# Kernel optimization log

Measured on AMD Instinct MI355X. Metric: run time of the kernel, lower is better.

## Reference

```python
import jax, jax.numpy as jnp
import numpy as np

N_NODES = 100000
N_EDGES = 1200000
D_IN = 64
H1 = 64
H2 = 64
N_CLASSES = 40
K_HOPS = 3  # PyG TAGConv default K=3


def _gcn_norm(edge_index, num_nodes):
    # TAGConv uses gcn_norm WITHOUT adding self-loops.
    src, dst = edge_index[0], edge_index[1]
    ones = jnp.ones((src.shape[0],), dtype=jnp.float32)
    deg = jax.ops.segment_sum(ones, dst, num_segments=num_nodes)
    deg_inv_sqrt = jnp.where(deg > 0, jax.lax.rsqrt(jnp.maximum(deg, 1.0)), 0.0)
    return deg_inv_sqrt[src] * deg_inv_sqrt[dst]  # [E]


def _tag_conv(x, src, dst, norm, W, b, num_nodes, K):
    # out = concat([x, Ax, ..., A^K x]) @ W + b, A = D^-1/2 A D^-1/2
    hops = [x]
    h = x
    for _ in range(K):
        h = jax.ops.segment_sum(h[src] * norm[:, None], dst, num_segments=num_nodes)
        hops.append(h)
    return jnp.concatenate(hops, axis=-1) @ W + b


def setup_inputs() -> dict:
    key = jax.random.key(0)
    ks = jax.random.split(key, 9)
    x = jax.random.normal(ks[0], (N_NODES, D_IN), dtype=jnp.float32)
    edge_index = jax.random.randint(ks[1], (2, N_EDGES), 0, N_NODES, dtype=jnp.int64)
    W1 = jax.random.normal(ks[2], ((K_HOPS + 1) * D_IN, H1), dtype=jnp.float32) * 0.05
    b1 = jnp.zeros((H1,), dtype=jnp.float32)
    W2 = jax.random.normal(ks[3], ((K_HOPS + 1) * H1, H2), dtype=jnp.float32) * 0.05
    b2 = jnp.zeros((H2,), dtype=jnp.float32)
    Wc = jax.random.normal(ks[4], (H2, N_CLASSES), dtype=jnp.float32) * 0.05
    bc = jnp.zeros((N_CLASSES,), dtype=jnp.float32)
    return {"x": x, "edge_index": edge_index, "W1": W1, "b1": b1,
            "W2": W2, "b2": b2, "Wc": Wc, "bc": bc}


def reference(x, edge_index, W1, b1, W2, b2, Wc, bc):
    num_nodes = x.shape[0]
    src, dst = edge_index[0], edge_index[1]
    norm = _gcn_norm(edge_index, num_nodes)
    h = _tag_conv(x, src, dst, norm, W1, b1, num_nodes, K_HOPS)
    h = jax.nn.relu(h)  # dropout is identity at inference
    h = _tag_conv(h, src, dst, norm, W2, b2, num_nodes, K_HOPS)
    h = jax.nn.relu(h)
    return h @ Wc + bc  # [N, num_classes]
```

## Files before the change

kernel.cpp:

```cpp
#include <hip/hip_runtime.h>
#include <hip/hip_bf16.h>
#include <stdint.h>

static constexpr int TG_NN = 100000;
static constexpr int TG_NE = 1200000;
static constexpr int TG_D  = 64;
static constexpr int TG_NC = 40;
static constexpr int TG_BT = 256;
static constexpr int TG_GN = (TG_NN + TG_BT - 1) / TG_BT;
static constexpr int TG_CAP = 64;
static constexpr int TG_WSH = 15;
static constexpr int TG_NPASS = (TG_NN + (1 << TG_WSH) - 1) >> TG_WSH;
static constexpr int TG_NR = TG_NN + 128;
static constexpr long TG_BS = (long)TG_NR * TG_D;

typedef __attribute__((ext_vector_type(8))) short tg71_s8;
typedef __attribute__((ext_vector_type(4))) float tg71_f4;

__device__ __forceinline__ float tg71_b2f(unsigned short u) {
    return __uint_as_float(((unsigned int)u) << 16);
}
__device__ __forceinline__ unsigned short tg71_f2b(float v) {
    __hip_bfloat16 b = __float2bfloat16(v);
    return __builtin_bit_cast(unsigned short, b);
}
__device__ __forceinline__ float tg71_ld(const void* p, long i, int isF32) {
    if (isF32) return ((const float*)p)[i];
    return tg71_b2f(((const unsigned short*)p)[i]);
}
__device__ __forceinline__ void tg71_st(void* p, long i, int isF32, float v) {
    if (isF32) ((float*)p)[i] = v;
    else ((unsigned short*)p)[i] = tg71_f2b(v);
}
__device__ __forceinline__ float4 tg71_u2f4(ushort4 u) {
    return float4{tg71_b2f(u.x), tg71_b2f(u.y), tg71_b2f(u.z), tg71_b2f(u.w)};
}

__global__ void tg71_detect(const int* ei, const unsigned short* w1bits, int* flags) {
    int lane = threadIdx.x;
    int hi = ei[2 * lane + 1];
    unsigned long long bi = __ballot(hi != 0);
    float mx = 0.0f;
    for (int k = lane; k < 2048; k += 64) {
        float v = fabsf(tg71_b2f(w1bits[k]));
        if (!(v == v)) v = 1e30f;
        mx = fmaxf(mx, v);
    }
    unsigned long long bf = __ballot(mx > 1e4f);
    if (lane == 0) { flags[0] = (bi == 0ULL) ? 1 : 0; flags[1] = (bf != 0ULL) ? 1 : 0; }
}

extern "C" __global__ void TAGModel_71227737636876_kernel(void* out, const int* flags) {
    long i = (long)blockIdx.x * blockDim.x + threadIdx.x;
    if (i < (long)TG_NN * TG_NC) tg71_st(out, i, flags[1], 123.0f);
}

__global__ void tg71_prep(const void* W1, const void* W2, const int* flags,
                          unsigned short* Wt1, unsigned short* Wt2, int* cnt,
                          unsigned short* Sall) {
    int b = blockIdx.x;
    if (b < 128) {
        const void* W = (b < 64) ? W1 : W2;
        unsigned short* Wt = (b < 64) ? Wt1 : Wt2;
        int i = (b & 63) * TG_BT + threadIdx.x;
        int k = i >> 6, n = i & 63;
        Wt[n * 256 + k] = flags[1] ? tg71_f2b(((const float*)W)[i]) : ((const unsigned short*)W)[i];
    } else if (b < 128 + TG_GN) {
        int i = (b - 128) * TG_BT + threadIdx.x;
        if (i < TG_NN) cnt[i] = 0;
    } else {
        int j = (b - 128 - TG_GN) * TG_BT + threadIdx.x;
        if (j < 5 * 2048) {
            int buf = j >> 11, w = j & 2047;
            unsigned short* base = Sall + (long)buf * TG_BS + (long)TG_NN * TG_D;
            ((uint2*)base)[w] = uint2{0u, 0u};
        }
    }
}

__global__ void tg71_scatter(const int* __restrict__ ei, const int* flags,
                             int* __restrict__ srcI, int* __restrict__ dstI,
                             int* cnt, int* __restrict__ srcS, int pass, int decode) {
    int e = blockIdx.x * blockDim.x + threadIdx.x;
    if (e >= TG_NE) return;
    int s, d;
    if (decode) {
        if (flags[0]) { s = ((const int2*)ei)[e].x; d = ((const int2*)ei)[TG_NE + e].x; }
        else          { s = ei[e]; d = ei[TG_NE + e]; }
        srcI[e] = s;
        dstI[e] = d;
    } else {
        s = srcI[e];
        d = dstI[e];
    }
    if ((d >> TG_WSH) != pass) return;
    int pos = atomicAdd(cnt + d, 1);
    if (pos < TG_CAP) srcS[(d << 6) + pos] = s;
}

__global__ void tg71_gx(const void* x, const int* flags, const int* __restrict__ cnt,
                        float* __restrict__ dis, unsigned short* __restrict__ g) {
    int tid = blockIdx.x * blockDim.x + threadIdx.x;
    if (tid >= TG_NN * 4) return;
    int n = tid >> 2, q = tid & 3;
    if (q == 0) {
        int c = cnt[n];
        dis[n] = c > 0 ? rsqrtf((float)c) : 0.f;
    }
    unsigned short* dst = g + (long)n * TG_D + q * 16;
    if (flags[1]) {
        const float* p = (const float*)x + (long)n * TG_D + q * 16;
        float4 v0 = *(const float4*)p, v1 = *(const float4*)(p + 4);
        float4 v2 = *(const float4*)(p + 8), v3 = *(const float4*)(p + 12);
        tg71_s8 o0, o1;
        o0[0] = (short)tg71_f2b(v0.x); o0[1] = (short)tg71_f2b(v0.y);
        o0[2] = (short)tg71_f2b(v0.z); o0[3] = (short)tg71_f2b(v0.w);
        o0[4] = (short)tg71_f2b(v1.x); o0[5] = (short)tg71_f2b(v1.y);
        o0[6] = (short)tg71_f2b(v1.z); o0[7] = (short)tg71_f2b(v1.w);
        o1[0] = (short)tg71_f2b(v2.x); o1[1] = (short)tg71_f2b(v2.y);
        o1[2] = (short)tg71_f2b(v2.z); o1[3] = (short)tg71_f2b(v2.w);
        o1[4] = (short)tg71_f2b(v3.x); o1[5] = (short)tg71_f2b(v3.y);
        o1[6] = (short)tg71_f2b(v3.z); o1[7] = (short)tg71_f2b(v3.w);
        *(tg71_s8*)dst = o0;
        *(tg71_s8*)(dst + 8) = o1;
    } else {
        const unsigned short* p = (const unsigned short*)x + (long)n * TG_D + q * 16;
        *(tg71_s8*)dst = *(const tg71_s8*)p;
        *(tg71_s8*)(dst + 8) = *(const tg71_s8*)(p + 8);
    }
}

__global__ void tg71_prop(const int* __restrict__ cnt, const int* __restrict__ srcS,
                          const float* __restrict__ dis,
                          const unsigned short* __restrict__ in,
                          unsigned short* __restrict__ out) {
    int gid = blockIdx.x * blockDim.x + threadIdx.x;
    int wid = gid >> 6, lane = gid & 63;
    int grp = lane >> 3, li = lane & 7;
    int n = wid * 8 + grp;
    int len = min(cnt[n], TG_CAP);
    int r0 = n << 6;
    long fo = (long)li * 8;

    int4 qa = *(const int4*)&srcS[r0];
    int4 qb = *(const int4*)&srcS[r0 + 4];
    int4 qc = *(const int4*)&srcS[r0 + 8];
    int4 qd = *(const int4*)&srcS[r0 + 12];
    int idx[16] = {qa.x, qa.y, qa.z, qa.w, qb.x, qb.y, qb.z, qb.w,
                   qc.x, qc.y, qc.z, qc.w, qd.x, qd.y, qd.z, qd.w};

    tg71_s8 w[16];
    float wgt[16];
#pragma unroll
    for (int j = 0; j < 16; ++j) {
        int aj = (j < len) ? idx[j] : 0;
        w[j] = *(const tg71_s8*)&in[(long)aj * TG_D + fo];
        wgt[j] = (j < len) ? dis[aj] : 0.f;
    }

    float acc[8];
#pragma unroll
    for (int f = 0; f < 8; ++f) acc[f] = 0.f;
#pragma unroll
    for (int j = 0; j < 16; ++j) {
#pragma unroll
        for (int f = 0; f < 8; ++f)
            acc[f] += wgt[j] * tg71_b2f((unsigned short)w[j][f]);
    }

    for (int k = 16; k < len; k += 8) {
        int4 ra = *(const int4*)&srcS[r0 + k];
        int4 rb = *(const int4*)&srcS[r0 + k + 4];
        int jdx[8] = {ra.x, ra.y, ra.z, ra.w, rb.x, rb.y, rb.z, rb.w};
        tg71_s8 v[8];
        float vw[8];
#pragma unroll
        for (int j = 0; j < 8; ++j) {
            int aj = (k + j < len) ? jdx[j] : 0;
            v[j] = *(const tg71_s8*)&in[(long)aj * TG_D + fo];
            vw[j] = (k + j < len) ? dis[aj] : 0.f;
        }
#pragma unroll
        for (int j = 0; j < 8; ++j) {
#pragma unroll
            for (int f = 0; f < 8; ++f)
                acc[f] += vw[j] * tg71_b2f((unsigned short)v[j][f]);
        }
    }

    float dn = dis[n];
    tg71_s8 oh;
#pragma unroll
    for (int f = 0; f < 8; ++f) oh[f] = (short)tg71_f2b(acc[f] * dn);
    *(tg71_s8*)&out[(long)n * TG_D + fo] = oh;
}

__global__ __launch_bounds__(256) void tg71_gemm(
    const unsigned short* A0, const unsigned short* A1, const unsigned short* A2,
    const unsigned short* A3, const unsigned short* Wt, const void* bias, const int* flags,
    unsigned short* yOut, int doHead, const void* Wc, const void* bc, void* outp) {
    __shared__ __align__(16) unsigned short sZ[128 * 68];
    __shared__ unsigned short sWc[41 * 68];

    const int t    = threadIdx.x;
    const int wave = t >> 6;
    const int lane = t & 63;
    const int quad = lane >> 4;
    const int lr   = lane & 15;
    const int fF   = flags[1];
    const long tile = (long)blockIdx.x * 128;
    const long row0 = tile + wave * 32 + lr;
    const long row1 = row0 + 16;

    const unsigned short* As[4] = {A0, A1, A2, A3};

    tg71_s8 af[4][2][2];
#pragma unroll
    for (int seg = 0; seg < 4; ++seg)
#pragma unroll
        for (int ks = 0; ks < 2; ++ks)
#pragma unroll
            for (int m = 0; m < 2; ++m)
                af[seg][ks][m] = *(const tg71_s8*)(As[seg] + (m ? row1 : row0) * TG_D +
                                                   ks * 32 + quad * 8);

    tg71_f4 acc[2][4];
#pragma unroll
    for (int mt = 0; mt < 2; ++mt)
#pragma unroll
        for (int nt = 0; nt < 4; ++nt) acc[mt][nt] = tg71_f4{0.f, 0.f, 0.f, 0.f};

#pragma unroll
    for (int seg = 0; seg < 4; ++seg)
#pragma unroll
        for (int ks = 0; ks < 2; ++ks) {
            const int kw = seg * 64 + ks * 32 + quad * 8;
            tg71_s8 b0 = *(const tg71_s8*)&Wt[(0  + lr) * 256 + kw];
            tg71_s8 b1 = *(const tg71_s8*)&Wt[(16 + lr) * 256 + kw];
            tg71_s8 b2 = *(const tg71_s8*)&Wt[(32 + lr) * 256 + kw];
            tg71_s8 b3 = *(const tg71_s8*)&Wt[(48 + lr) * 256 + kw];
            const tg71_s8 a0 = af[seg][ks][0];
            const tg71_s8 a1 = af[seg][ks][1];
            acc[0][0] = __builtin_amdgcn_mfma_f32_16x16x32_bf16(a0, b0, acc[0][0], 0, 0, 0);
            acc[0][1] = __builtin_amdgcn_mfma_f32_16x16x32_bf16(a0, b1, acc[0][1], 0, 0, 0);
            acc[0][2] = __builtin_amdgcn_mfma_f32_16x16x32_bf16(a0, b2, acc[0][2], 0, 0, 0);
            acc[0][3] = __builtin_amdgcn_mfma_f32_16x16x32_bf16(a0, b3, acc[0][3], 0, 0, 0);
            acc[1][0] = __builtin_amdgcn_mfma_f32_16x16x32_bf16(a1, b0, acc[1][0], 0, 0, 0);
            acc[1][1] = __builtin_amdgcn_mfma_f32_16x16x32_bf16(a1, b1, acc[1][1], 0, 0, 0);
            acc[1][2] = __builtin_amdgcn_mfma_f32_16x16x32_bf16(a1, b2, acc[1][2], 0, 0, 0);
            acc[1][3] = __builtin_amdgcn_mfma_f32_16x16x32_bf16(a1, b3, acc[1][3], 0, 0, 0);
        }

    float bv[4];
#pragma unroll
    for (int nt = 0; nt < 4; ++nt) bv[nt] = tg71_ld(bias, nt * 16 + lr, fF);

#pragma unroll
    for (int mt = 0; mt < 2; ++mt) {
#pragma unroll
        for (int r = 0; r < 4; ++r) {
            int ml = wave * 32 + mt * 16 + quad * 4 + r;
#pragma unroll
            for (int nt = 0; nt < 4; ++nt) {
                float v = fmaxf(acc[mt][nt][r] + bv[nt], 0.f);
                sZ[ml * 68 + nt * 16 + lr] = tg71_f2b(v);
            }
        }
    }

    if (!doHead) {
        __syncthreads();
        for (int c = t; c < 2048; c += 256) {
            int m = c >> 4, f4 = (c & 15) * 4;
            *(ushort4*)&yOut[(tile + m) * TG_D + f4] = *(const ushort4*)&sZ[m * 68 + f4];
        }
        return;
    }

    for (int i = t; i < 64 * TG_NC; i += 256) {
        int f = i / TG_NC, c = i - f * TG_NC;
        sWc[c * 68 + f] = fF ? tg71_f2b(((const float*)Wc)[i]) : ((const unsigned short*)Wc)[i];
    }
    if (t < TG_NC) sWc[40 * 68 + t] = fF ? tg71_f2b(((const float*)bc)[t]) : ((const unsigned short*)bc)[t];
    __syncthreads();

    const int jb = t & 7;
    const int mb = t >> 3;
    float hacc[4][5];
#pragma unroll
    for (int i = 0; i < 4; ++i)
#pragma unroll
        for (int q = 0; q < 5; ++q) hacc[i][q] = 0.f;
    for (int fc = 0; fc < 64; fc += 4) {
        float4 zv[4], wv[5];
#pragma unroll
        for (int i = 0; i < 4; ++i)
            zv[i] = tg71_u2f4(*(const ushort4*)&sZ[(mb + 32 * i) * 68 + fc]);
#pragma unroll
        for (int q = 0; q < 5; ++q)
            wv[q] = tg71_u2f4(*(const ushort4*)&sWc[(jb * 5 + q) * 68 + fc]);
#pragma unroll
        for (int i = 0; i < 4; ++i)
#pragma unroll
            for (int q = 0; q < 5; ++q)
                hacc[i][q] += zv[i].x * wv[q].x + zv[i].y * wv[q].y +
                              zv[i].z * wv[q].z + zv[i].w * wv[q].w;
    }
#pragma unroll
    for (int i = 0; i < 4; ++i) {
        long n = tile + mb + 32 * i;
        if (n < TG_NN) {
#pragma unroll
            for (int q = 0; q < 5; ++q) {
                int c = jb * 5 + q;
                tg71_st(outp, n * TG_NC + c, fF, hacc[i][q] + tg71_b2f(sWc[40 * 68 + c]));
            }
        }
    }
}

extern "C" void kernel_launch(void* const* d_in, const int* in_sizes, int n_in,
                              void* d_out, int out_size, void* d_ws, size_t ws_size,
                              hipStream_t stream) {
    const void* x  = d_in[0];
    const int*  ei = (const int*)d_in[1];
    const void* W1 = d_in[2];
    const void* b1 = d_in[3];
    const void* W2 = d_in[4];
    const void* b2 = d_in[5];
    const void* Wc = d_in[6];
    const void* bc = d_in[7];

    int*   flags = (int*)d_ws;
    int*   srcI  = flags + 16;
    int*   dstI  = srcI + TG_NE;
    int*   cnt   = dstI + TG_NE;
    float* dis   = (float*)(cnt + TG_NN);
    int*   srcS  = (int*)(dis + TG_NN);
    unsigned short* Sall = (unsigned short*)(((uintptr_t)(srcS + TG_NN * TG_CAP) + 255) &
                                             ~(uintptr_t)255);
    unsigned short* S1 = Sall + 0 * TG_BS;
    unsigned short* S2 = Sall + 1 * TG_BS;
    unsigned short* S3 = Sall + 2 * TG_BS;
    unsigned short* S4 = Sall + 3 * TG_BS;
    unsigned short* S5 = Sall + 4 * TG_BS;
    unsigned short* Wt1 = Sall + 5 * TG_BS;
    unsigned short* Wt2 = Wt1 + 64 * 256;

    const int gE = (TG_NE + TG_BT - 1) / TG_BT;
    const int gP = TG_NN / 32;
    const int gX = (TG_NN * 4 + TG_BT - 1) / TG_BT;
    const int gT = (TG_NN + 127) / 128;

    tg71_detect<<<1, 64, 0, stream>>>(ei, (const unsigned short*)W1, flags);
    tg71_prep<<<128 + TG_GN + 40, TG_BT, 0, stream>>>(W1, W2, flags, Wt1, Wt2, cnt, Sall);

    for (int pass = 0; pass < TG_NPASS; ++pass)
        tg71_scatter<<<gE, TG_BT, 0, stream>>>(ei, flags, srcI, dstI, cnt, srcS,
                                               pass, pass == 0 ? 1 : 0);

    tg71_gx<<<gX, TG_BT, 0, stream>>>(x, flags, cnt, dis, S1);
    tg71_prop<<<gP, TG_BT, 0, stream>>>(cnt, srcS, dis, S1, S2);
    tg71_prop<<<gP, TG_BT, 0, stream>>>(cnt, srcS, dis, S2, S3);
    tg71_prop<<<gP, TG_BT, 0, stream>>>(cnt, srcS, dis, S3, S4);
    tg71_gemm<<<gT, TG_BT, 0, stream>>>(S1, S2, S3, S4, Wt1, b1, flags,
                                        S5, 0, nullptr, nullptr, nullptr);

    tg71_prop<<<gP, TG_BT, 0, stream>>>(cnt, srcS, dis, S5, S2);
    tg71_prop<<<gP, TG_BT, 0, stream>>>(cnt, srcS, dis, S2, S3);
    tg71_prop<<<gP, TG_BT, 0, stream>>>(cnt, srcS, dis, S3, S4);
    tg71_gemm<<<gT, TG_BT, 0, stream>>>(S5, S2, S3, S4, Wt2, b2, flags,
                                        nullptr, 1, Wc, bc, d_out);
}
```

Baseline: 399.7 us.

## Halve scatter passes, drop decoded index copies, stage GEMM weights in LDS

The destination window shift rises from 15 to 16, so the edge scatter needs 2 passes over the edges instead of 4. Each pass now reads the edge index directly instead of first writing decoded src/dst arrays, which removes 2.4M int writes and reads. The GEMM kernel copies the transposed weight tile into shared memory, reusing the output staging buffer, and reads B fragments from LDS instead of global memory. This adds two block barriers and a larger shared allocation per block, which may lower occupancy.

```diff
diff --git a/kernel.cpp b/kernel.cpp
--- a/kernel.cpp
+++ b/kernel.cpp
@@ -9,7 +9,7 @@
 static constexpr int TG_BT = 256;
 static constexpr int TG_GN = (TG_NN + TG_BT - 1) / TG_BT;
 static constexpr int TG_CAP = 64;
-static constexpr int TG_WSH = 15;
+static constexpr int TG_WSH = 16;
 static constexpr int TG_NPASS = (TG_NN + (1 << TG_WSH) - 1) >> TG_WSH;
 static constexpr int TG_NR = TG_NN + 128;
 static constexpr long TG_BS = (long)TG_NR * TG_D;
@@ -79,20 +79,12 @@
 }
 
 __global__ void tg71_scatter(const int* __restrict__ ei, const int* flags,
-                             int* __restrict__ srcI, int* __restrict__ dstI,
-                             int* cnt, int* __restrict__ srcS, int pass, int decode) {
+                             int* cnt, int* __restrict__ srcS, int pass) {
     int e = blockIdx.x * blockDim.x + threadIdx.x;
     if (e >= TG_NE) return;
     int s, d;
-    if (decode) {
-        if (flags[0]) { s = ((const int2*)ei)[e].x; d = ((const int2*)ei)[TG_NE + e].x; }
-        else          { s = ei[e]; d = ei[TG_NE + e]; }
-        srcI[e] = s;
-        dstI[e] = d;
-    } else {
-        s = srcI[e];
-        d = dstI[e];
-    }
+    if (flags[0]) { s = ((const int2*)ei)[e].x; d = ((const int2*)ei)[TG_NE + e].x; }
+    else          { s = ei[e]; d = ei[TG_NE + e]; }
     if ((d >> TG_WSH) != pass) return;
     int pos = atomicAdd(cnt + d, 1);
     if (pos < TG_CAP) srcS[(d << 6) + pos] = s;
@@ -199,8 +191,10 @@
     const unsigned short* A0, const unsigned short* A1, const unsigned short* A2,
     const unsigned short* A3, const unsigned short* Wt, const void* bias, const int* flags,
     unsigned short* yOut, int doHead, const void* Wc, const void* bc, void* outp) {
-    __shared__ __align__(16) unsigned short sZ[128 * 68];
+    __shared__ __align__(16) unsigned short sU[64 * 256];
     __shared__ unsigned short sWc[41 * 68];
+    unsigned short* sWt = sU;
+    unsigned short* sZ  = sU;
 
     const int t    = threadIdx.x;
     const int wave = t >> 6;
@@ -224,6 +218,13 @@
                 af[seg][ks][m] = *(const tg71_s8*)(As[seg] + (m ? row1 : row0) * TG_D +
                                                    ks * 32 + quad * 8);
 
+    for (int u = t; u < 2048; u += 256) {
+        int n = u & 63, k8 = u >> 6;
+        tg71_s8 v = *(const tg71_s8*)&Wt[n * 256 + k8 * 8];
+        *(tg71_s8*)&sWt[k8 * 512 + n * 8] = v;
+    }
+    __syncthreads();
+
     tg71_f4 acc[2][4];
 #pragma unroll
     for (int mt = 0; mt < 2; ++mt)
@@ -234,11 +235,12 @@
     for (int seg = 0; seg < 4; ++seg)
 #pragma unroll
         for (int ks = 0; ks < 2; ++ks) {
-            const int kw = seg * 64 + ks * 32 + quad * 8;
-            tg71_s8 b0 = *(const tg71_s8*)&Wt[(0  + lr) * 256 + kw];
-            tg71_s8 b1 = *(const tg71_s8*)&Wt[(16 + lr) * 256 + kw];
-            tg71_s8 b2 = *(const tg71_s8*)&Wt[(32 + lr) * 256 + kw];
-            tg71_s8 b3 = *(const tg71_s8*)&Wt[(48 + lr) * 256 + kw];
+            const int k8v = seg * 8 + ks * 4 + quad;
+            const unsigned short* bb = &sWt[k8v * 512 + lr * 8];
+            tg71_s8 b0 = *(const tg71_s8*)(bb);
+            tg71_s8 b1 = *(const tg71_s8*)(bb + 128);
+            tg71_s8 b2 = *(const tg71_s8*)(bb + 256);
+            tg71_s8 b3 = *(const tg71_s8*)(bb + 384);
             const tg71_s8 a0 = af[seg][ks][0];
             const tg71_s8 a1 = af[seg][ks][1];
             acc[0][0] = __builtin_amdgcn_mfma_f32_16x16x32_bf16(a0, b0, acc[0][0], 0, 0, 0);
@@ -250,6 +252,8 @@
             acc[1][2] = __builtin_amdgcn_mfma_f32_16x16x32_bf16(a1, b2, acc[1][2], 0, 0, 0);
             acc[1][3] = __builtin_amdgcn_mfma_f32_16x16x32_bf16(a1, b3, acc[1][3], 0, 0, 0);
         }
+
+    __syncthreads();
 
     float bv[4];
 #pragma unroll
@@ -332,9 +336,7 @@
     const void* bc = d_in[7];
 
     int*   flags = (int*)d_ws;
-    int*   srcI  = flags + 16;
-    int*   dstI  = srcI + TG_NE;
-    int*   cnt   = dstI + TG_NE;
+    int*   cnt   = flags + 16;
     float* dis   = (float*)(cnt + TG_NN);
     int*   srcS  = (int*)(dis + TG_NN);
     unsigned short* Sall = (unsigned short*)(((uintptr_t)(srcS + TG_NN * TG_CAP) + 255) &
@@ -356,8 +358,7 @@
     tg71_prep<<<128 + TG_GN + 40, TG_BT, 0, stream>>>(W1, W2, flags, Wt1, Wt2, cnt, Sall);
 
     for (int pass = 0; pass < TG_NPASS; ++pass)
-        tg71_scatter<<<gE, TG_BT, 0, stream>>>(ei, flags, srcI, dstI, cnt, srcS,
-                                               pass, pass == 0 ? 1 : 0);
+        tg71_scatter<<<gE, TG_BT, 0, stream>>>(ei, flags, cnt, srcS, pass);
 
     tg71_gx<<<gX, TG_BT, 0, stream>>>(x, flags, cnt, dis, S1);
     tg71_prop<<<gP, TG_BT, 0, stream>>>(cnt, srcS, dis, S1, S2);
```

Measured after the change: 382.6 us. 1.04x faster.
